# Kernel optimization log

Measured on AMD Instinct MI355X. Metric: run time of the kernel, lower is better.

The kernel has to match this reference:

```python
import jax, jax.numpy as jnp
import numpy as np

DIM = 1024
NUM_HEADS = 16
HEAD_DIM = DIM // NUM_HEADS  # 64
BATCH = 4
SEQ = 2048


def setup_inputs() -> dict:
    key = jax.random.key(0)
    ks = jax.random.split(key, 7)
    bound = 1.0 / np.sqrt(HEAD_DIM)
    linear_embed = jax.random.normal(ks[0], (BATCH, SEQ, DIM), dtype=jnp.float32)
    # torch nn.Linear weights are [out, in]; stacked per head -> [H, hd, hd]
    Wq = jax.random.uniform(ks[1], (NUM_HEADS, HEAD_DIM, HEAD_DIM), jnp.float32, -bound, bound)
    bq = jax.random.uniform(ks[2], (NUM_HEADS, HEAD_DIM), jnp.float32, -bound, bound)
    Wk = jax.random.uniform(ks[3], (NUM_HEADS, HEAD_DIM, HEAD_DIM), jnp.float32, -bound, bound)
    bk = jax.random.uniform(ks[4], (NUM_HEADS, HEAD_DIM), jnp.float32, -bound, bound)
    Wv = jax.random.uniform(ks[5], (NUM_HEADS, HEAD_DIM, HEAD_DIM), jnp.float32, -bound, bound)
    bv = jax.random.uniform(ks[6], (NUM_HEADS, HEAD_DIM), jnp.float32, -bound, bound)
    return {"linear_embed": linear_embed, "Wq": Wq, "bq": bq, "Wk": Wk, "bk": bk, "Wv": Wv, "bv": bv}


def reference(linear_embed, Wq, bq, Wk, bk, Wv, bv):
    # Faithful to the original bug: output.append is outside the image loop,
    # so only the LAST image's attention result is returned, shape [1, S, dim].
    x = linear_embed[-1]                      # [S, dim]
    S = x.shape[0]
    xh = x.reshape(S, NUM_HEADS, HEAD_DIM)    # per-head slices of the feature dim
    # Linear: y = x @ W.T + b  (W is [out, in])
    q = jnp.einsum('shd,hed->hse', xh, Wq) + bq[:, None, :]   # [H, S, hd]
    k = jnp.einsum('shd,hed->hse', xh, Wk) + bk[:, None, :]
    v = jnp.einsum('shd,hed->hse', xh, Wv) + bv[:, None, :]
    scale = 1.0 / np.sqrt(HEAD_DIM).astype(np.float32)
    scores = jnp.einsum('hse,hte->hst', q, k) * scale          # [H, S, S]
    attn = jax.nn.softmax(scores, axis=-1)
    out = jnp.einsum('hst,hte->hse', attn, v)                  # [H, S, hd]
    out = jnp.transpose(out, (1, 0, 2)).reshape(S, NUM_HEADS * HEAD_DIM)  # hstack heads
    return out[None]                                           # [1, S, dim]
```

## Files before the change

### kernel.cpp

```cpp
#include <hip/hip_runtime.h>


#define NUM_HEADS 16
#define HEAD_DIM  64
#define SEQ       2048
#define DIM       1024
#define BATCH     4

typedef unsigned short u16;
typedef unsigned int   u32;
typedef __bf16 bf16x8 __attribute__((ext_vector_type(8)));
typedef float  f32x4  __attribute__((ext_vector_type(4)));

#define QSCALE (0.125f * 1.44269504088896340736f)

__device__ __forceinline__ u16 f2bf(float f) {
  u32 u = __builtin_bit_cast(u32, f);
  u += 0x7FFFu + ((u >> 16) & 1u);
  return (u16)(u >> 16);
}

__device__ __forceinline__ bf16x8 as_frag(uint4 v) {
  return __builtin_bit_cast(bf16x8, v);
}

__device__ __forceinline__ f32x4 mfma16(bf16x8 a, bf16x8 b, f32x4 c) {
  return __builtin_amdgcn_mfma_f32_16x16x32_bf16(a, b, c, 0, 0, 0);
}

__device__ __forceinline__ void gload16(const void* g, void* l) {
  __builtin_amdgcn_global_load_lds(
      (const __attribute__((address_space(1))) void*)g,
      (__attribute__((address_space(3))) void*)l, 16, 0, 0);
}

__global__ __launch_bounds__(256) void proj_kernel(
    const float* __restrict__ x,
    const float* __restrict__ Wq, const float* __restrict__ bq,
    const float* __restrict__ Wk, const float* __restrict__ bk,
    const float* __restrict__ Wv, const float* __restrict__ bv,
    u16* __restrict__ qb, u16* __restrict__ kb, u16* __restrict__ vT)
{
  const int bid = blockIdx.x;
  const int h   = bid & 15;
  const int st0 = (bid >> 4) * 128;
  const int tid  = threadIdx.x;
  const int w    = tid >> 6;
  const int lane = tid & 63;
  const int g    = lane >> 4;
  const int c    = lane & 15;

  __shared__ __align__(16) u16 xl[128 * 64];
  __shared__ __align__(16) u16 wl[3][64 * 64];

#pragma unroll
  for (int it = 0; it < 8; ++it) {
    int idx  = tid + it * 256;
    int row  = idx >> 4;
    int col4 = idx & 15;
    float4 f = *(const float4*)(x + (size_t)(st0 + row) * DIM + h * HEAD_DIM + col4 * 4);
    ushort4 b;
    b.x = f2bf(f.x); b.y = f2bf(f.y); b.z = f2bf(f.z); b.w = f2bf(f.w);
    int byte = row * 128 + (((col4 >> 1) ^ (row & 7)) << 4) + (col4 & 1) * 8;
    *(ushort4*)((char*)xl + byte) = b;
  }
  const float* const Ws[3] = {Wq + (size_t)h * 4096, Wk + (size_t)h * 4096, Wv + (size_t)h * 4096};
#pragma unroll
  for (int it = 0; it < 12; ++it) {
    const int mat = it >> 2;
    int rem  = tid + (it & 3) * 256;
    int row  = rem >> 4;
    int col4 = rem & 15;
    float4 f = *(const float4*)(Ws[mat] + row * HEAD_DIM + col4 * 4);
    ushort4 b;
    b.x = f2bf(f.x); b.y = f2bf(f.y); b.z = f2bf(f.z); b.w = f2bf(f.w);
    int byte = row * 128 + (((col4 >> 1) ^ (row & 7)) << 4) + (col4 & 1) * 8;
    *(ushort4*)((char*)wl[mat] + byte) = b;
  }
  __syncthreads();

  bf16x8 xa[2][2];
#pragma unroll
  for (int rt = 0; rt < 2; ++rt)
#pragma unroll
    for (int ch = 0; ch < 2; ++ch) {
      int rl = w * 32 + rt * 16 + c;
      int byte = rl * 128 + ((((ch << 2) + g) ^ (c & 7)) << 4);
      xa[rt][ch] = as_frag(*(const uint4*)((const char*)xl + byte));
    }

#pragma unroll
  for (int mat = 0; mat < 2; ++mat) {
    const float* bias = (mat == 0) ? bq : bk;
    u16* dst = (mat == 0) ? qb : kb;
#pragma unroll
    for (int eb = 0; eb < 4; ++eb) {
      bf16x8 wb[2];
#pragma unroll
      for (int ch = 0; ch < 2; ++ch) {
        int e = eb * 16 + c;
        int byte = e * 128 + ((((ch << 2) + g) ^ (c & 7)) << 4);
        wb[ch] = as_frag(*(const uint4*)((const char*)wl[mat] + byte));
      }
      float bval = bias[h * HEAD_DIM + eb * 16 + c];
#pragma unroll
      for (int rt = 0; rt < 2; ++rt) {
        f32x4 acc = {0.f, 0.f, 0.f, 0.f};
        acc = mfma16(xa[rt][0], wb[0], acc);
        acc = mfma16(xa[rt][1], wb[1], acc);
#pragma unroll
        for (int i = 0; i < 4; ++i) {
          float v = acc[i] + bval;
          if (mat == 0) v *= QSCALE;
          int srow = st0 + w * 32 + rt * 16 + g * 4 + i;
          dst[((size_t)h * SEQ + srow) * HEAD_DIM + eb * 16 + c] = f2bf(v);
        }
      }
    }
  }

#pragma unroll
  for (int eb = 0; eb < 4; ++eb) {
    bf16x8 wa[2];
#pragma unroll
    for (int ch = 0; ch < 2; ++ch) {
      int e = eb * 16 + c;
      int byte = e * 128 + ((((ch << 2) + g) ^ (c & 7)) << 4);
      wa[ch] = as_frag(*(const uint4*)((const char*)wl[2] + byte));
    }
    float bvv[4];
#pragma unroll
    for (int i = 0; i < 4; ++i) bvv[i] = bv[h * HEAD_DIM + eb * 16 + g * 4 + i];
#pragma unroll
    for (int rt = 0; rt < 2; ++rt) {
      f32x4 acc = {0.f, 0.f, 0.f, 0.f};
      acc = mfma16(wa[0], xa[rt][0], acc);
      acc = mfma16(wa[1], xa[rt][1], acc);
#pragma unroll
      for (int i = 0; i < 4; ++i) {
        int e = eb * 16 + g * 4 + i;
        vT[((size_t)h * HEAD_DIM + e) * SEQ + st0 + w * 32 + rt * 16 + c] =
            f2bf(acc[i] + bvv[i]);
      }
    }
  }
}

__global__ __launch_bounds__(256) void attn_kernel(
    const u16* __restrict__ qb, const u16* __restrict__ kb,
    const u16* __restrict__ vT, float* __restrict__ out)
{
  const int bid = blockIdx.x;
  const int h   = bid & 15;
  const int s0  = (bid >> 4) * 128;
  const int tid  = threadIdx.x;
  const int w    = tid >> 6;
  const int lane = tid & 63;
  const int g    = lane >> 4;
  const int c    = lane & 15;
  const int sw   = s0 + w * 32;

  __shared__ __align__(16) char kbuf[2][8192];
  __shared__ __align__(16) char vbuf[2][8192];

  const u16* kbh = kb + (size_t)h * SEQ * HEAD_DIM;
  const u16* vth = vT + (size_t)h * HEAD_DIM * SEQ;

  bf16x8 qf[2][2];
#pragma unroll
  for (int rt = 0; rt < 2; ++rt)
#pragma unroll
    for (int ch = 0; ch < 2; ++ch)
      qf[rt][ch] = as_frag(*(const uint4*)(
          qb + ((size_t)h * SEQ + sw + rt * 16 + c) * HEAD_DIM + ch * 32 + g * 8));

  f32x4 acc[2][4] = {};
  float m_[2] = {-3e38f, -3e38f};
  float l_[2] = {0.f, 0.f};

  auto stage = [&](int buf, int t0) {
#pragma unroll
    for (int q2 = 0; q2 < 2; ++q2) {
      int u  = (w * 2 + q2) * 64 + lane;
      int rr = u >> 3;
      int sl = u & 7;
      const char* gk = (const char*)(kbh + (size_t)(t0 + rr) * HEAD_DIM) +
                       ((sl ^ (rr & 7)) << 4);
      gload16(gk, &kbuf[buf][(w * 2 + q2) * 1024]);
      const char* gv = (const char*)(vth + (size_t)rr * SEQ + t0) +
                       ((sl ^ (rr & 7)) << 4);
      gload16(gv, &vbuf[buf][(w * 2 + q2) * 1024]);
    }
  };

  stage(0, 0);
  __syncthreads();

  int cur = 0;
  for (int t = 0; t < SEQ / 64; ++t) {
    if (t < SEQ / 64 - 1) stage(cur ^ 1, (t + 1) * 64);

    f32x4 st_[2][4];
#pragma unroll
    for (int tb = 0; tb < 4; ++tb) {
      bf16x8 ka0, ka1;
      {
        int rr = tb * 16 + c;
        int b0 = rr * 128 + (((0 + g) ^ (c & 7)) << 4);
        int b1 = rr * 128 + (((4 + g) ^ (c & 7)) << 4);
        ka0 = as_frag(*(const uint4*)(kbuf[cur] + b0));
        ka1 = as_frag(*(const uint4*)(kbuf[cur] + b1));
      }
#pragma unroll
      for (int rt = 0; rt < 2; ++rt) {
        f32x4 z = {0.f, 0.f, 0.f, 0.f};
        z = mfma16(ka0, qf[rt][0], z);
        st_[rt][tb] = mfma16(ka1, qf[rt][1], z);
      }
    }

    u32 pk[2][8];
#pragma unroll
    for (int rt = 0; rt < 2; ++rt) {
      float mt = -3e38f;
#pragma unroll
      for (int tb = 0; tb < 4; ++tb)
#pragma unroll
        for (int i = 0; i < 4; ++i) mt = fmaxf(mt, st_[rt][tb][i]);
      mt = fmaxf(mt, __shfl_xor(mt, 16));
      mt = fmaxf(mt, __shfl_xor(mt, 32));
      float mn = fmaxf(m_[rt], mt);
      float al = exp2f(m_[rt] - mn);
      float p[4][4];
      float rs = 0.f;
#pragma unroll
      for (int tb = 0; tb < 4; ++tb)
#pragma unroll
        for (int i = 0; i < 4; ++i) {
          p[tb][i] = exp2f(st_[rt][tb][i] - mn);
          rs += p[tb][i];
        }
      rs += __shfl_xor(rs, 16);
      rs += __shfl_xor(rs, 32);
      l_[rt] = l_[rt] * al + rs;
      m_[rt] = mn;
#pragma unroll
      for (int eb = 0; eb < 4; ++eb) acc[rt][eb] *= al;
#pragma unroll
      for (int tb = 0; tb < 4; ++tb) {
        pk[rt][tb * 2 + 0] = (u32)f2bf(p[tb][0]) | ((u32)f2bf(p[tb][1]) << 16);
        pk[rt][tb * 2 + 1] = (u32)f2bf(p[tb][2]) | ((u32)f2bf(p[tb][3]) << 16);
      }
    }

#pragma unroll
    for (int eb = 0; eb < 4; ++eb) {
      int e = eb * 16 + c;
#pragma unroll
      for (int k0 = 0; k0 < 2; ++k0) {
        int b0 = e * 128 + ((((k0 << 2) + 0 + (g >> 1)) ^ (c & 7)) << 4) + (g & 1) * 8;
        int b1 = e * 128 + ((((k0 << 2) + 2 + (g >> 1)) ^ (c & 7)) << 4) + (g & 1) * 8;
        uint2 lo = *(const uint2*)(vbuf[cur] + b0);
        uint2 hi = *(const uint2*)(vbuf[cur] + b1);
        bf16x8 va = as_frag(make_uint4(lo.x, lo.y, hi.x, hi.y));
#pragma unroll
        for (int rt = 0; rt < 2; ++rt) {
          bf16x8 pf = as_frag(make_uint4(pk[rt][k0 * 4 + 0], pk[rt][k0 * 4 + 1],
                                         pk[rt][k0 * 4 + 2], pk[rt][k0 * 4 + 3]));
          acc[rt][eb] = mfma16(va, pf, acc[rt][eb]);
        }
      }
    }

    __syncthreads();
    cur ^= 1;
  }

#pragma unroll
  for (int rt = 0; rt < 2; ++rt) {
    float rinv = 1.0f / l_[rt];
#pragma unroll
    for (int eb = 0; eb < 4; ++eb) {
      float4 o;
      o.x = acc[rt][eb][0] * rinv;
      o.y = acc[rt][eb][1] * rinv;
      o.z = acc[rt][eb][2] * rinv;
      o.w = acc[rt][eb][3] * rinv;
      *(float4*)(out + (size_t)(sw + rt * 16 + c) * DIM + h * HEAD_DIM +
                 eb * 16 + g * 4) = o;
    }
  }
}

extern "C" void kernel_launch(void* const* d_in, const int* in_sizes, int n_in,
                              void* d_out, int out_size, void* d_ws, size_t ws_size,
                              hipStream_t stream) {
  const float* le = (const float*)d_in[0];
  const float* x  = le + (size_t)(BATCH - 1) * SEQ * DIM;
  const float* Wq = (const float*)d_in[1];
  const float* bq = (const float*)d_in[2];
  const float* Wk = (const float*)d_in[3];
  const float* bk = (const float*)d_in[4];
  const float* Wv = (const float*)d_in[5];
  const float* bv = (const float*)d_in[6];

  u16* qb = (u16*)d_ws;
  u16* kb = qb + (size_t)NUM_HEADS * SEQ * HEAD_DIM;
  u16* vT = kb + (size_t)NUM_HEADS * SEQ * HEAD_DIM;

  proj_kernel<<<256, 256, 0, stream>>>(x, Wq, bq, Wk, bk, Wv, bv, qb, kb, vT);
  attn_kernel<<<256, 256, 0, stream>>>(qb, kb, vT, (float*)d_out);
}
```

Baseline: 160.6 us.

## Halve query tile per block to double grid size and occupancy

Both the projection and attention kernels now process 64 query rows per block instead of 128, so each wave handles 16 rows and the launch grows from 256 to 512 blocks. With 256 blocks on a chip with 256 CUs the GPU was underfilled, so doubling the grid and adding launch_bounds(256,2) is meant to raise occupancy and latency hiding. The attention loop is unrolled by two with fixed buffer indices, precomputed LDS offsets and pointer-increment staging. The projection kernel writes packed 8-byte bf16 stores. The trade-off is that each K/V tile loaded into LDS now serves half as many query rows, doubling total K/V traffic.

```diff
diff --git a/kernel.cpp b/kernel.cpp
--- a/kernel.cpp
+++ b/kernel.cpp
@@ -1,11 +1,10 @@
 #include <hip/hip_runtime.h>
 
 
-#define NUM_HEADS 16
-#define HEAD_DIM  64
-#define SEQ       2048
-#define DIM       1024
-#define BATCH     4
+#define NH  16
+#define HD  64
+#define SEQ 2048
+#define DIM 1024
 
 typedef unsigned short u16;
 typedef unsigned int   u32;
@@ -19,15 +18,13 @@
   u += 0x7FFFu + ((u >> 16) & 1u);
   return (u16)(u >> 16);
 }
-
-__device__ __forceinline__ bf16x8 as_frag(uint4 v) {
-  return __builtin_bit_cast(bf16x8, v);
-}
-
+__device__ __forceinline__ u32 pkbf(float a, float b) {
+  return (u32)f2bf(a) | ((u32)f2bf(b) << 16);
+}
+__device__ __forceinline__ bf16x8 as_frag(uint4 v) { return __builtin_bit_cast(bf16x8, v); }
 __device__ __forceinline__ f32x4 mfma16(bf16x8 a, bf16x8 b, f32x4 c) {
   return __builtin_amdgcn_mfma_f32_16x16x32_bf16(a, b, c, 0, 0, 0);
 }
-
 __device__ __forceinline__ void gload16(const void* g, void* l) {
   __builtin_amdgcn_global_load_lds(
       (const __attribute__((address_space(1))) void*)g,
@@ -43,51 +40,52 @@
 {
   const int bid = blockIdx.x;
   const int h   = bid & 15;
-  const int st0 = (bid >> 4) * 128;
+  const int st0 = (bid >> 4) * 64;
   const int tid  = threadIdx.x;
   const int w    = tid >> 6;
   const int lane = tid & 63;
   const int g    = lane >> 4;
   const int c    = lane & 15;
 
-  __shared__ __align__(16) u16 xl[128 * 64];
+  __shared__ __align__(16) u16 xl[64 * 64];
   __shared__ __align__(16) u16 wl[3][64 * 64];
 
 #pragma unroll
-  for (int it = 0; it < 8; ++it) {
-    int idx  = tid + it * 256;
-    int row  = idx >> 4;
-    int col4 = idx & 15;
-    float4 f = *(const float4*)(x + (size_t)(st0 + row) * DIM + h * HEAD_DIM + col4 * 4);
-    ushort4 b;
-    b.x = f2bf(f.x); b.y = f2bf(f.y); b.z = f2bf(f.z); b.w = f2bf(f.w);
+  for (int it = 0; it < 4; ++it) {
+    int u    = tid + it * 256;
+    int row  = u >> 4;
+    int col4 = u & 15;
+    float4 f = *(const float4*)(x + (size_t)(st0 + row) * DIM + h * HD + col4 * 4);
     int byte = row * 128 + (((col4 >> 1) ^ (row & 7)) << 4) + (col4 & 1) * 8;
-    *(ushort4*)((char*)xl + byte) = b;
-  }
-  const float* const Ws[3] = {Wq + (size_t)h * 4096, Wk + (size_t)h * 4096, Wv + (size_t)h * 4096};
+    uint2 pkd;
+    pkd.x = pkbf(f.x, f.y);
+    pkd.y = pkbf(f.z, f.w);
+    *(uint2*)((char*)xl + byte) = pkd;
+  }
+  const float* const Ws[3] = {Wq + (size_t)h * 4096, Wk + (size_t)h * 4096,
+                              Wv + (size_t)h * 4096};
 #pragma unroll
   for (int it = 0; it < 12; ++it) {
     const int mat = it >> 2;
-    int rem  = tid + (it & 3) * 256;
-    int row  = rem >> 4;
-    int col4 = rem & 15;
-    float4 f = *(const float4*)(Ws[mat] + row * HEAD_DIM + col4 * 4);
-    ushort4 b;
-    b.x = f2bf(f.x); b.y = f2bf(f.y); b.z = f2bf(f.z); b.w = f2bf(f.w);
+    int u    = tid + (it & 3) * 256;
+    int row  = u >> 4;
+    int col4 = u & 15;
+    float4 f = *(const float4*)(Ws[mat] + row * HD + col4 * 4);
     int byte = row * 128 + (((col4 >> 1) ^ (row & 7)) << 4) + (col4 & 1) * 8;
-    *(ushort4*)((char*)wl[mat] + byte) = b;
+    uint2 pkd;
+    pkd.x = pkbf(f.x, f.y);
+    pkd.y = pkbf(f.z, f.w);
+    *(uint2*)((char*)wl[mat] + byte) = pkd;
   }
   __syncthreads();
 
-  bf16x8 xa[2][2];
-#pragma unroll
-  for (int rt = 0; rt < 2; ++rt)
-#pragma unroll
-    for (int ch = 0; ch < 2; ++ch) {
-      int rl = w * 32 + rt * 16 + c;
-      int byte = rl * 128 + ((((ch << 2) + g) ^ (c & 7)) << 4);
-      xa[rt][ch] = as_frag(*(const uint4*)((const char*)xl + byte));
-    }
+  bf16x8 xa[2];
+#pragma unroll
+  for (int ch = 0; ch < 2; ++ch) {
+    int byte = (w * 16 + c) * 128 + ((((ch << 2) + g) ^ (c & 7)) << 4);
+    xa[ch] = as_frag(*(const uint4*)((const char*)xl + byte));
+  }
+  const int sbase = st0 + w * 16;
 
 #pragma unroll
   for (int mat = 0; mat < 2; ++mat) {
@@ -95,200 +93,190 @@
     u16* dst = (mat == 0) ? qb : kb;
 #pragma unroll
     for (int eb = 0; eb < 4; ++eb) {
-      bf16x8 wb[2];
-#pragma unroll
-      for (int ch = 0; ch < 2; ++ch) {
-        int e = eb * 16 + c;
-        int byte = e * 128 + ((((ch << 2) + g) ^ (c & 7)) << 4);
-        wb[ch] = as_frag(*(const uint4*)((const char*)wl[mat] + byte));
-      }
-      float bval = bias[h * HEAD_DIM + eb * 16 + c];
-#pragma unroll
-      for (int rt = 0; rt < 2; ++rt) {
-        f32x4 acc = {0.f, 0.f, 0.f, 0.f};
-        acc = mfma16(xa[rt][0], wb[0], acc);
-        acc = mfma16(xa[rt][1], wb[1], acc);
-#pragma unroll
-        for (int i = 0; i < 4; ++i) {
-          float v = acc[i] + bval;
-          if (mat == 0) v *= QSCALE;
-          int srow = st0 + w * 32 + rt * 16 + g * 4 + i;
-          dst[((size_t)h * SEQ + srow) * HEAD_DIM + eb * 16 + c] = f2bf(v);
-        }
-      }
+      bf16x8 wf0, wf1;
+      {
+        int b0 = (eb * 16 + c) * 128 + (((0 + g) ^ (c & 7)) << 4);
+        int b1 = (eb * 16 + c) * 128 + (((4 + g) ^ (c & 7)) << 4);
+        wf0 = as_frag(*(const uint4*)((const char*)wl[mat] + b0));
+        wf1 = as_frag(*(const uint4*)((const char*)wl[mat] + b1));
+      }
+      float4 b4 = *(const float4*)(bias + h * HD + eb * 16 + g * 4);
+      f32x4 acc = {0.f, 0.f, 0.f, 0.f};
+      acc = mfma16(wf0, xa[0], acc);
+      acc = mfma16(wf1, xa[1], acc);
+      float v0 = acc[0] + b4.x, v1 = acc[1] + b4.y;
+      float v2 = acc[2] + b4.z, v3 = acc[3] + b4.w;
+      if (mat == 0) { v0 *= QSCALE; v1 *= QSCALE; v2 *= QSCALE; v3 *= QSCALE; }
+      uint2 st;
+      st.x = pkbf(v0, v1);
+      st.y = pkbf(v2, v3);
+      *(uint2*)(dst + ((size_t)h * SEQ + sbase + c) * HD + eb * 16 + g * 4) = st;
     }
   }
 
 #pragma unroll
   for (int eb = 0; eb < 4; ++eb) {
-    bf16x8 wa[2];
-#pragma unroll
-    for (int ch = 0; ch < 2; ++ch) {
-      int e = eb * 16 + c;
-      int byte = e * 128 + ((((ch << 2) + g) ^ (c & 7)) << 4);
-      wa[ch] = as_frag(*(const uint4*)((const char*)wl[2] + byte));
+    bf16x8 wf0, wf1;
+    {
+      int b0 = (eb * 16 + c) * 128 + (((0 + g) ^ (c & 7)) << 4);
+      int b1 = (eb * 16 + c) * 128 + (((4 + g) ^ (c & 7)) << 4);
+      wf0 = as_frag(*(const uint4*)((const char*)wl[2] + b0));
+      wf1 = as_frag(*(const uint4*)((const char*)wl[2] + b1));
     }
-    float bvv[4];
-#pragma unroll
-    for (int i = 0; i < 4; ++i) bvv[i] = bv[h * HEAD_DIM + eb * 16 + g * 4 + i];
-#pragma unroll
-    for (int rt = 0; rt < 2; ++rt) {
-      f32x4 acc = {0.f, 0.f, 0.f, 0.f};
-      acc = mfma16(wa[0], xa[rt][0], acc);
-      acc = mfma16(wa[1], xa[rt][1], acc);
-#pragma unroll
-      for (int i = 0; i < 4; ++i) {
-        int e = eb * 16 + g * 4 + i;
-        vT[((size_t)h * HEAD_DIM + e) * SEQ + st0 + w * 32 + rt * 16 + c] =
-            f2bf(acc[i] + bvv[i]);
-      }
-    }
-  }
-}
-
-__global__ __launch_bounds__(256) void attn_kernel(
+    float bvv = bv[h * HD + eb * 16 + c];
+    f32x4 acc = {0.f, 0.f, 0.f, 0.f};
+    acc = mfma16(xa[0], wf0, acc);
+    acc = mfma16(xa[1], wf1, acc);
+    uint2 st;
+    st.x = pkbf(acc[0] + bvv, acc[1] + bvv);
+    st.y = pkbf(acc[2] + bvv, acc[3] + bvv);
+    *(uint2*)(vT + ((size_t)h * HD + eb * 16 + c) * SEQ + sbase + g * 4) = st;
+  }
+}
+
+__global__ __launch_bounds__(256, 2) void attn_kernel(
     const u16* __restrict__ qb, const u16* __restrict__ kb,
     const u16* __restrict__ vT, float* __restrict__ out)
 {
-  const int bid = blockIdx.x;
-  const int h   = bid & 15;
-  const int s0  = (bid >> 4) * 128;
+  const int bid  = blockIdx.x;
+  const int h    = bid & 15;
+  const int qt   = bid >> 4;
   const int tid  = threadIdx.x;
   const int w    = tid >> 6;
   const int lane = tid & 63;
   const int g    = lane >> 4;
   const int c    = lane & 15;
-  const int sw   = s0 + w * 32;
+  const int sw   = qt * 64 + w * 16;
 
   __shared__ __align__(16) char kbuf[2][8192];
   __shared__ __align__(16) char vbuf[2][8192];
 
-  const u16* kbh = kb + (size_t)h * SEQ * HEAD_DIM;
-  const u16* vth = vT + (size_t)h * HEAD_DIM * SEQ;
-
-  bf16x8 qf[2][2];
-#pragma unroll
-  for (int rt = 0; rt < 2; ++rt)
+  const u16* kbh = kb + (size_t)h * SEQ * HD;
+  const u16* vth = vT + (size_t)h * HD * SEQ;
+
+  bf16x8 qf[2];
+#pragma unroll
+  for (int ch = 0; ch < 2; ++ch)
+    qf[ch] = as_frag(*(const uint4*)(
+        qb + ((size_t)h * SEQ + sw + c) * HD + ch * 32 + g * 8));
+
+  int qkoff[4][2];
+#pragma unroll
+  for (int tb = 0; tb < 4; ++tb)
 #pragma unroll
     for (int ch = 0; ch < 2; ++ch)
-      qf[rt][ch] = as_frag(*(const uint4*)(
-          qb + ((size_t)h * SEQ + sw + rt * 16 + c) * HEAD_DIM + ch * 32 + g * 8));
-
-  f32x4 acc[2][4] = {};
-  float m_[2] = {-3e38f, -3e38f};
-  float l_[2] = {0.f, 0.f};
-
-  auto stage = [&](int buf, int t0) {
-#pragma unroll
-    for (int q2 = 0; q2 < 2; ++q2) {
-      int u  = (w * 2 + q2) * 64 + lane;
-      int rr = u >> 3;
-      int sl = u & 7;
-      const char* gk = (const char*)(kbh + (size_t)(t0 + rr) * HEAD_DIM) +
-                       ((sl ^ (rr & 7)) << 4);
-      gload16(gk, &kbuf[buf][(w * 2 + q2) * 1024]);
-      const char* gv = (const char*)(vth + (size_t)rr * SEQ + t0) +
-                       ((sl ^ (rr & 7)) << 4);
-      gload16(gv, &vbuf[buf][(w * 2 + q2) * 1024]);
+      qkoff[tb][ch] = (tb * 16 + c) * 128 + ((((ch << 2) + g) ^ (c & 7)) << 4);
+  int pvoff[4][2][2];
+#pragma unroll
+  for (int eb = 0; eb < 4; ++eb)
+#pragma unroll
+    for (int k0 = 0; k0 < 2; ++k0) {
+      pvoff[eb][k0][0] = (eb * 16 + c) * 128 +
+                         ((((k0 << 2) + 0 + (g >> 1)) ^ (c & 7)) << 4) + (g & 1) * 8;
+      pvoff[eb][k0][1] = (eb * 16 + c) * 128 +
+                         ((((k0 << 2) + 2 + (g >> 1)) ^ (c & 7)) << 4) + (g & 1) * 8;
     }
+
+  const int u1 = w * 128 + lane, u2 = u1 + 64;
+  const int rr1 = u1 >> 3, sl1 = u1 & 7, rr2 = u2 >> 3, sl2 = u2 & 7;
+  const char* gk1 = (const char*)kbh + rr1 * 128 + ((sl1 ^ (rr1 & 7)) << 4);
+  const char* gk2 = (const char*)kbh + rr2 * 128 + ((sl2 ^ (rr2 & 7)) << 4);
+  const char* gv1 = (const char*)vth + rr1 * 4096 + ((sl1 ^ (rr1 & 7)) << 4);
+  const char* gv2 = (const char*)vth + rr2 * 4096 + ((sl2 ^ (rr2 & 7)) << 4);
+  char* kd1 = (char*)kbuf + u1 * 16;
+  char* kd2 = (char*)kbuf + u2 * 16;
+  char* vd1 = (char*)vbuf + u1 * 16;
+  char* vd2 = (char*)vbuf + u2 * 16;
+  auto stage = [&](int buf) {
+    int bo = buf * 8192;
+    gload16(gk1, kd1 + bo);
+    gload16(gk2, kd2 + bo);
+    gload16(gv1, vd1 + bo);
+    gload16(gv2, vd2 + bo);
+    gk1 += 8192; gk2 += 8192; gv1 += 128; gv2 += 128;
   };
 
-  stage(0, 0);
+  f32x4 acc[4] = {};
+  float m_ = -3e38f;
+  float l_ = 0.f;
+
+  stage(0);
   __syncthreads();
 
-  int cur = 0;
-  for (int t = 0; t < SEQ / 64; ++t) {
-    if (t < SEQ / 64 - 1) stage(cur ^ 1, (t + 1) * 64);
-
-    f32x4 st_[2][4];
-#pragma unroll
-    for (int tb = 0; tb < 4; ++tb) {
-      bf16x8 ka0, ka1;
-      {
-        int rr = tb * 16 + c;
-        int b0 = rr * 128 + (((0 + g) ^ (c & 7)) << 4);
-        int b1 = rr * 128 + (((4 + g) ^ (c & 7)) << 4);
-        ka0 = as_frag(*(const uint4*)(kbuf[cur] + b0));
-        ka1 = as_frag(*(const uint4*)(kbuf[cur] + b1));
-      }
-#pragma unroll
-      for (int rt = 0; rt < 2; ++rt) {
+  for (int t = 0; t < 32; t += 2) {
+#pragma unroll
+    for (int tt = 0; tt < 2; ++tt) {
+      if (t + tt + 1 < 32) stage(tt ^ 1);
+
+      f32x4 st_[4];
+#pragma unroll
+      for (int tb = 0; tb < 4; ++tb) {
+        bf16x8 ka0 = as_frag(*(const uint4*)(kbuf[tt] + qkoff[tb][0]));
+        bf16x8 ka1 = as_frag(*(const uint4*)(kbuf[tt] + qkoff[tb][1]));
         f32x4 z = {0.f, 0.f, 0.f, 0.f};
-        z = mfma16(ka0, qf[rt][0], z);
-        st_[rt][tb] = mfma16(ka1, qf[rt][1], z);
-      }
-    }
-
-    u32 pk[2][8];
-#pragma unroll
-    for (int rt = 0; rt < 2; ++rt) {
+        z = mfma16(ka0, qf[0], z);
+        st_[tb] = mfma16(ka1, qf[1], z);
+      }
+
       float mt = -3e38f;
 #pragma unroll
       for (int tb = 0; tb < 4; ++tb)
 #pragma unroll
-        for (int i = 0; i < 4; ++i) mt = fmaxf(mt, st_[rt][tb][i]);
+        for (int i = 0; i < 4; ++i) mt = fmaxf(mt, st_[tb][i]);
       mt = fmaxf(mt, __shfl_xor(mt, 16));
       mt = fmaxf(mt, __shfl_xor(mt, 32));
-      float mn = fmaxf(m_[rt], mt);
-      float al = exp2f(m_[rt] - mn);
+      float mn = fmaxf(m_, mt);
+      float al = exp2f(m_ - mn);
       float p[4][4];
       float rs = 0.f;
 #pragma unroll
       for (int tb = 0; tb < 4; ++tb)
 #pragma unroll
         for (int i = 0; i < 4; ++i) {
-          p[tb][i] = exp2f(st_[rt][tb][i] - mn);
+          p[tb][i] = exp2f(st_[tb][i] - mn);
           rs += p[tb][i];
         }
       rs += __shfl_xor(rs, 16);
       rs += __shfl_xor(rs, 32);
-      l_[rt] = l_[rt] * al + rs;
-      m_[rt] = mn;
-#pragma unroll
-      for (int eb = 0; eb < 4; ++eb) acc[rt][eb] *= al;
+      l_ = l_ * al + rs;
+      m_ = mn;
+#pragma unroll
+      for (int eb = 0; eb < 4; ++eb) {
+        acc[eb][0] *= al; acc[eb][1] *= al;
+        acc[eb][2] *= al; acc[eb][3] *= al;
+      }
+      u32 pk[8];
 #pragma unroll
       for (int tb = 0; tb < 4; ++tb) {
-        pk[rt][tb * 2 + 0] = (u32)f2bf(p[tb][0]) | ((u32)f2bf(p[tb][1]) << 16);
-        pk[rt][tb * 2 + 1] = (u32)f2bf(p[tb][2]) | ((u32)f2bf(p[tb][3]) << 16);
-      }
+        pk[tb * 2 + 0] = pkbf(p[tb][0], p[tb][1]);
+        pk[tb * 2 + 1] = pkbf(p[tb][2], p[tb][3]);
+      }
+
+#pragma unroll
+      for (int eb = 0; eb < 4; ++eb) {
+#pragma unroll
+        for (int k0 = 0; k0 < 2; ++k0) {
+          uint2 lo = *(const uint2*)(vbuf[tt] + pvoff[eb][k0][0]);
+          uint2 hi = *(const uint2*)(vbuf[tt] + pvoff[eb][k0][1]);
+          bf16x8 va = as_frag(make_uint4(lo.x, lo.y, hi.x, hi.y));
+          bf16x8 pf = as_frag(make_uint4(pk[k0 * 4 + 0], pk[k0 * 4 + 1],
+                                         pk[k0 * 4 + 2], pk[k0 * 4 + 3]));
+          acc[eb] = mfma16(va, pf, acc[eb]);
+        }
+      }
+
+      __syncthreads();
     }
-
-#pragma unroll
-    for (int eb = 0; eb < 4; ++eb) {
-      int e = eb * 16 + c;
-#pragma unroll
-      for (int k0 = 0; k0 < 2; ++k0) {
-        int b0 = e * 128 + ((((k0 << 2) + 0 + (g >> 1)) ^ (c & 7)) << 4) + (g & 1) * 8;
-        int b1 = e * 128 + ((((k0 << 2) + 2 + (g >> 1)) ^ (c & 7)) << 4) + (g & 1) * 8;
-        uint2 lo = *(const uint2*)(vbuf[cur] + b0);
-        uint2 hi = *(const uint2*)(vbuf[cur] + b1);
-        bf16x8 va = as_frag(make_uint4(lo.x, lo.y, hi.x, hi.y));
-#pragma unroll
-        for (int rt = 0; rt < 2; ++rt) {
-          bf16x8 pf = as_frag(make_uint4(pk[rt][k0 * 4 + 0], pk[rt][k0 * 4 + 1],
-                                         pk[rt][k0 * 4 + 2], pk[rt][k0 * 4 + 3]));
-          acc[rt][eb] = mfma16(va, pf, acc[rt][eb]);
-        }
-      }
-    }
-
-    __syncthreads();
-    cur ^= 1;
-  }
-
-#pragma unroll
-  for (int rt = 0; rt < 2; ++rt) {
-    float rinv = 1.0f / l_[rt];
-#pragma unroll
-    for (int eb = 0; eb < 4; ++eb) {
-      float4 o;
-      o.x = acc[rt][eb][0] * rinv;
-      o.y = acc[rt][eb][1] * rinv;
-      o.z = acc[rt][eb][2] * rinv;
-      o.w = acc[rt][eb][3] * rinv;
-      *(float4*)(out + (size_t)(sw + rt * 16 + c) * DIM + h * HEAD_DIM +
-                 eb * 16 + g * 4) = o;
-    }
+  }
+
+  const int s = sw + c;
+  float rinv = 1.0f / l_;
+#pragma unroll
+  for (int eb = 0; eb < 4; ++eb) {
+    float4 o;
+    o.x = acc[eb][0] * rinv; o.y = acc[eb][1] * rinv;
+    o.z = acc[eb][2] * rinv; o.w = acc[eb][3] * rinv;
+    *(float4*)(out + (size_t)s * DIM + h * HD + eb * 16 + g * 4) = o;
   }
 }
 
@@ -296,7 +284,7 @@
                               void* d_out, int out_size, void* d_ws, size_t ws_size,
                               hipStream_t stream) {
   const float* le = (const float*)d_in[0];
-  const float* x  = le + (size_t)(BATCH - 1) * SEQ * DIM;
+  const float* x  = le + (size_t)3 * SEQ * DIM;
   const float* Wq = (const float*)d_in[1];
   const float* bq = (const float*)d_in[2];
   const float* Wk = (const float*)d_in[3];
@@ -305,9 +293,9 @@
   const float* bv = (const float*)d_in[6];
 
   u16* qb = (u16*)d_ws;
-  u16* kb = qb + (size_t)NUM_HEADS * SEQ * HEAD_DIM;
-  u16* vT = kb + (size_t)NUM_HEADS * SEQ * HEAD_DIM;
-
-  proj_kernel<<<256, 256, 0, stream>>>(x, Wq, bq, Wk, bk, Wv, bv, qb, kb, vT);
-  attn_kernel<<<256, 256, 0, stream>>>(qb, kb, vT, (float*)d_out);
-}
+  u16* kb = qb + (size_t)NH * SEQ * HD;
+  u16* vT = kb + (size_t)NH * SEQ * HD;
+
+  proj_kernel<<<512, 256, 0, stream>>>(x, Wq, bq, Wk, bk, Wv, bv, qb, kb, vT);
+  attn_kernel<<<512, 256, 0, stream>>>(qb, kb, vT, (float*)d_out);
+}
```

Measured after the change: 136.9 us. 1.17x faster.
